# Kernel optimization log

Hardware: AMD Instinct MI355X
Metric: run time of the kernel (lower is better)

## Reference

```python
import jax, jax.numpy as jnp
import numpy as np

EPS = 1e-10
NCE_T = 0.1
JSD_T = 1.0

def setup_inputs() -> dict:
    key = jax.random.key(0)
    k1, k2, k3, k4, k5 = jax.random.split(key, 5)
    N, D, C = 8192, 128, 1000
    return {
        'fs': jax.random.normal(k1, (N, D), dtype=jnp.float32),
        'ft': jax.random.normal(k2, (N, D), dtype=jnp.float32),
        'logit_s': jax.random.normal(k3, (N, C), dtype=jnp.float32),
        'logit_t': jax.random.normal(k4, (N, C), dtype=jnp.float32),
        'target': jax.random.randint(k5, (N,), 0, 100, dtype=jnp.int64),
    }

def _l2_normalize(x, axis=1, eps=1e-12):
    n = jnp.sqrt(jnp.sum(x * x, axis=axis, keepdims=True))
    return x / jnp.maximum(n, eps)

def _nce_loss(f1, f2, targets):
    f1 = _l2_normalize(f1)
    f2 = _l2_normalize(f2)
    # pos_mask[i,j] = 1 where targets[i] == targets[j] (same class, incl. diagonal)
    pos_mask = (targets[:, None] == targets[None, :]).astype(jnp.float32)  # [N,N]
    neg_mask = 1.0 - pos_mask
    # dist = ||f1_i - f2_j||^2 = 2 - 2 <f1_i, f2_j> for unit vectors -> cos = 1 - 0.5*dist = f1 @ f2.T
    cos = jnp.matmul(f1, f2.T)  # [N,N]
    ps = jax.nn.softmax(cos / NCE_T, axis=1)
    log_pos = -jnp.log(ps + EPS) * pos_mask
    log_neg = -jnp.log(1.0 - ps + EPS) * neg_mask
    row = log_pos.sum(1) / pos_mask.sum(1) + log_neg.sum(1) / neg_mask.sum(1)
    return row.mean()

def _jsd_loss(y_s, y_t):
    N = y_s.shape[0]
    log_ps = jax.nn.log_softmax(y_s / JSD_T, axis=1)
    log_pt = jax.nn.log_softmax(y_t / JSD_T, axis=1)
    pt = jnp.exp(log_pt)
    ps = jnp.exp(log_ps)
    # F.kl_div(input=log_p, target=q, reduction='sum') = sum(q * (log q - log_p))
    kl_st = jnp.sum(pt * (log_pt - log_ps)) * (JSD_T ** 2) / N
    kl_ts = jnp.sum(ps * (log_ps - log_pt)) * (JSD_T ** 2) / N
    return 0.5 * (kl_st + kl_ts)

def reference(fs, ft, logit_s, logit_t, target):
    return _nce_loss(fs, ft, target) + _jsd_loss(logit_s, logit_t)
```

## Files before the change

kernel.cpp:

```cpp
#include <hip/hip_runtime.h>
#include <hip/hip_bf16.h>

#define NN 8192
#define DD 128
#define CC 1000
#define LN2 0.69314718f
#define G_SCALE 14.42695041f
#define NSTRIP 16
#define JPER   512
#define NTILE  8
#define LROW   128
#define GRID_MAIN 1024
#define RED_BLOCKS 32

typedef short v8s __attribute__((ext_vector_type(8)));
typedef float v4f __attribute__((ext_vector_type(4)));
typedef unsigned short u16;
typedef unsigned int u32;

typedef __attribute__((address_space(1))) const unsigned char ga_t;
typedef __attribute__((address_space(3))) unsigned char la_t;
#define GLOAD_LDS16(g, l) __builtin_amdgcn_global_load_lds((ga_t*)(g), (la_t*)(l), 16, 0, 0)

#if __has_builtin(__builtin_amdgcn_exp2f)
#define EXP2(x) __builtin_amdgcn_exp2f(x)
#else
#define EXP2(x) exp2f(x)
#endif
#if __has_builtin(__builtin_amdgcn_logf)
#define LOG2(x) __builtin_amdgcn_logf(x)
#else
#define LOG2(x) log2f(x)
#endif

static __device__ __forceinline__ float bf2f(u16 u) {
    union { float f; u32 i; } x; x.i = ((u32)u) << 16; return x.f;
}
static __device__ __forceinline__ u16 f2bf(float f) {
    u32 x = __float_as_uint(f);
    return (u16)((x + 0x7FFFu + ((x >> 16) & 1u)) >> 16);
}
static __device__ __forceinline__ float wsum(float v) {
    #pragma unroll
    for (int m = 1; m < 64; m <<= 1) v += __shfl_xor(v, m, 64);
    return v;
}
static __device__ __forceinline__ float wmax(float v) {
    #pragma unroll
    for (int m = 1; m < 64; m <<= 1) v = fmaxf(v, __shfl_xor(v, m, 64));
    return v;
}

__global__ __launch_bounds__(256) void prep_kernel(const void* __restrict__ fs,
                                                   const void* __restrict__ ft,
                                                   const int* __restrict__ traw,
                                                   u16* __restrict__ f1, u16* __restrict__ f2,
                                                   int* __restrict__ tgt32,
                                                   int* __restrict__ ghist,
                                                   float* __restrict__ sums) {
    __shared__ int h[128];
    int b = blockIdx.x, tid = threadIdx.x;
    int w = tid >> 6, lane = tid & 63;

    if (b < 1024) {
        #pragma unroll
        for (int r = 0; r < 4; r++) {
            int row4 = b * 16 + w * 4 + r;
            const void* src; u16* dst; float gain; int row;
            if (row4 < NN) { src = fs; dst = f1; gain = G_SCALE; row = row4; }
            else           { src = ft; dst = f2; gain = 1.0f;    row = row4 - NN; }
            u32 wb = ((const u32*)src)[(size_t)row * 64 + lane];
            unsigned e = (wb >> 7) & 0xFF;
            int isF32 = (__popcll(__ballot(e >= 100 && e <= 140)) < 32);
            float x0, x1;
            if (isF32) {
                float2 v = ((const float2*)src)[(size_t)row * 64 + lane];
                x0 = v.x; x1 = v.y;
            } else {
                x0 = bf2f((u16)(wb & 0xFFFF));
                x1 = bf2f((u16)(wb >> 16));
            }
            float ss = wsum(x0 * x0 + x1 * x1);
            float sc = gain / fmaxf(sqrtf(ss), 1e-12f);
            u32 outw = (u32)f2bf(x0 * sc) | ((u32)f2bf(x1 * sc) << 16);
            ((u32*)dst)[(size_t)row * 64 + lane] = outw;
        }
    } else {
        if (tid < 4) sums[tid] = 0.0f;
        if (tid < 128) h[tid] = 0;
        __syncthreads();
        for (int r = 0; r < 32; r++) {
            int idx = r * 256 + tid;
            int k = (idx >> 1) & 4095;
            int odd = traw[2 * k + 1];
            int is32 = (__ballot(odd != 0) != 0ull);
            int t = (is32 ? traw[idx] : traw[2 * idx]) & 127;
            tgt32[idx] = t;
            atomicAdd(&h[t], 1);
        }
        __syncthreads();
        if (tid < 128) ghist[tid] = h[tid];
    }
}

__global__ __launch_bounds__(256) void main_kernel(const u16* __restrict__ f1,
                                                   const u16* __restrict__ f2,
                                                   const int* __restrict__ tgt,
                                                   const void* __restrict__ ls,
                                                   const void* __restrict__ lt,
                                                   float* __restrict__ Pp,
                                                   float* __restrict__ Qp,
                                                   float* __restrict__ Sp,
                                                   float* __restrict__ sums) {
    __shared__ u16 lds[2][64 * LROW];
    __shared__ float sred[4];
    int bx = blockIdx.x;
    int tid = threadIdx.x;
    int w = tid >> 6, lane = tid & 63;

    {
        int strip = bx & (NSTRIP - 1);
        int ib = bx >> 4;
        int quad = lane >> 4, lcol = lane & 15;
        int ibase = ib * 128 + w * 32;

        v8s a0[4], a1[4];
        #pragma unroll
        for (int t = 0; t < 4; t++) {
            int k = t * 32 + quad * 8;
            a0[t] = *(const v8s*)(f1 + (size_t)(ibase + lcol) * DD + k);
            a1[t] = *(const v8s*)(f1 + (size_t)(ibase + 16 + lcol) * DD + k);
        }
        int ti[8];
        #pragma unroll
        for (int a = 0; a < 2; a++)
            #pragma unroll
            for (int v = 0; v < 4; v++)
                ti[a * 4 + v] = tgt[ibase + a * 16 + quad * 4 + v];

        float P[8] = {}, Q[8] = {}, S[8] = {};

        int rrl = 4 * w + (lane >> 4);
        int cg = (lane & 15) ^ rrl;
        const u16* gb = f2 + (size_t)strip * JPER * DD + (size_t)rrl * DD + cg * 8;
        int ldsbase = 4 * w * 256;

        #pragma unroll
        for (int r = 0; r < 4; r++)
            GLOAD_LDS16(gb + (size_t)r * 16 * DD,
                        (unsigned char*)lds[0] + ldsbase + r * 16 * 256);

        for (int it = 0; it < NTILE; ++it) {
            __syncthreads();
            if (it + 1 < NTILE) {
                const u16* g2 = gb + (size_t)(it + 1) * 64 * DD;
                unsigned char* l2 = (unsigned char*)lds[(it + 1) & 1] + ldsbase;
                #pragma unroll
                for (int r = 0; r < 4; r++)
                    GLOAD_LDS16(g2 + (size_t)r * 16 * DD, l2 + r * 16 * 256);
            }
            int jb = strip * JPER + it * 64;
            int tj0 = tgt[jb + lcol];
            int tj1 = tgt[jb + 16 + lcol];
            int tj2 = tgt[jb + 32 + lcol];
            int tj3 = tgt[jb + 48 + lcol];

            const u16* buf = lds[it & 1];
            v4f zero = {0.f, 0.f, 0.f, 0.f};
            v4f acc[8] = {zero, zero, zero, zero, zero, zero, zero, zero};
            #pragma unroll
            for (int t = 0; t < 4; t++) {
                int s = ((quad + 4 * t) ^ lcol) * 8;
                v8s b0 = *(const v8s*)(buf + (lcol)*LROW + s);
                v8s b1 = *(const v8s*)(buf + (16 + lcol) * LROW + s);
                v8s b2 = *(const v8s*)(buf + (32 + lcol) * LROW + s);
                v8s b3 = *(const v8s*)(buf + (48 + lcol) * LROW + s);
                acc[0] = __builtin_amdgcn_mfma_f32_16x16x32_bf16(a0[t], b0, acc[0], 0, 0, 0);
                acc[1] = __builtin_amdgcn_mfma_f32_16x16x32_bf16(a0[t], b1, acc[1], 0, 0, 0);
                acc[2] = __builtin_amdgcn_mfma_f32_16x16x32_bf16(a0[t], b2, acc[2], 0, 0, 0);
                acc[3] = __builtin_amdgcn_mfma_f32_16x16x32_bf16(a0[t], b3, acc[3], 0, 0, 0);
                acc[4] = __builtin_amdgcn_mfma_f32_16x16x32_bf16(a1[t], b0, acc[4], 0, 0, 0);
                acc[5] = __builtin_amdgcn_mfma_f32_16x16x32_bf16(a1[t], b1, acc[5], 0, 0, 0);
                acc[6] = __builtin_amdgcn_mfma_f32_16x16x32_bf16(a1[t], b2, acc[6], 0, 0, 0);
                acc[7] = __builtin_amdgcn_mfma_f32_16x16x32_bf16(a1[t], b3, acc[7], 0, 0, 0);
            }
            #pragma unroll
            for (int a = 0; a < 2; a++) {
                #pragma unroll
                for (int v = 0; v < 4; v++) {
                    int t_i = ti[a * 4 + v];
                    #pragma unroll
                    for (int jf = 0; jf < 4; jf++) {
                        float s2 = acc[a * 4 + jf][v];
                        float e1 = EXP2(s2);
                        int tj = (jf == 0) ? tj0 : (jf == 1) ? tj1 : (jf == 2) ? tj2 : tj3;
                        bool pos = (tj == t_i);
                        P[a * 4 + v] += e1;
                        Q[a * 4 + v] += pos ? e1 : 0.0f;
                        S[a * 4 + v] += pos ? s2 : 0.0f;
                    }
                }
            }
        }

        #pragma unroll
        for (int a = 0; a < 2; a++) {
            #pragma unroll
            for (int v = 0; v < 4; v++) {
                float p = P[a * 4 + v], q = Q[a * 4 + v], s = S[a * 4 + v];
                #pragma unroll
                for (int m = 1; m < 16; m <<= 1) {
                    p += __shfl_xor(p, m, 64);
                    q += __shfl_xor(q, m, 64);
                    s += __shfl_xor(s, m, 64);
                }
                if (lcol == 0) {
                    size_t idx = (size_t)strip * NN + ibase + a * 16 + quad * 4 + v;
                    Pp[idx] = p;
                    Qp[idx] = q;
                    Sp[idx] = s;
                }
            }
        }
    }

    float jacc = 0.0f;
    for (int jj = 0; jj < 2; jj++) {
        int row = bx * 8 + jj * 4 + w;
        u32 wb = ((const u32*)ls)[(size_t)row * 500 + lane];
        unsigned e = (wb >> 7) & 0xFF;
        int isF32 = (__popcll(__ballot(e >= 100 && e <= 140)) < 32);

        float xs[16], xt[16];
        #pragma unroll
        for (int c = 0; c < 4; c++) {
            int idx = c * 256 + lane * 4;
            if (idx < CC) {
                if (isF32) {
                    float4 a = *(const float4*)((const float*)ls + (size_t)row * CC + idx);
                    float4 bb = *(const float4*)((const float*)lt + (size_t)row * CC + idx);
                    xs[c*4+0] = a.x; xs[c*4+1] = a.y; xs[c*4+2] = a.z; xs[c*4+3] = a.w;
                    xt[c*4+0] = bb.x; xt[c*4+1] = bb.y; xt[c*4+2] = bb.z; xt[c*4+3] = bb.w;
                } else {
                    ushort4 a = *(const ushort4*)((const u16*)ls + (size_t)row * CC + idx);
                    ushort4 bb = *(const ushort4*)((const u16*)lt + (size_t)row * CC + idx);
                    xs[c*4+0] = bf2f(a.x); xs[c*4+1] = bf2f(a.y); xs[c*4+2] = bf2f(a.z); xs[c*4+3] = bf2f(a.w);
                    xt[c*4+0] = bf2f(bb.x); xt[c*4+1] = bf2f(bb.y); xt[c*4+2] = bf2f(bb.z); xt[c*4+3] = bf2f(bb.w);
                }
            } else {
                #pragma unroll
                for (int q = 0; q < 4; q++) { xs[c*4+q] = -1e30f; xt[c*4+q] = -1e30f; }
            }
        }
        #pragma unroll
        for (int q = 0; q < 16; q++) {
            asm volatile("" : "+v"(xs[q]));
            asm volatile("" : "+v"(xt[q]));
        }
        float ms = -1e30f, mt = -1e30f;
        #pragma unroll
        for (int q = 0; q < 16; q++) { ms = fmaxf(ms, xs[q]); mt = fmaxf(mt, xt[q]); }
        ms = wmax(ms); mt = wmax(mt);
        float es = 0.f, et = 0.f;
        #pragma unroll
        for (int q = 0; q < 16; q++) { es += __expf(xs[q] - ms); et += __expf(xt[q] - mt); }
        es = wsum(es); et = wsum(et);
        float lse_s = ms + __logf(es), lse_t = mt + __logf(et);
        float contrib = 0.f;
        #pragma unroll
        for (int q = 0; q < 16; q++) {
            float lps = xs[q] - lse_s, lpt = xt[q] - lse_t;
            contrib += (lpt - lps) * (__expf(lpt) - __expf(lps));
        }
        jacc += contrib;
    }
    jacc = wsum(jacc);
    if (lane == 0) sred[w] = jacc;
    __syncthreads();
    if (tid == 0) atomicAdd(&sums[1], sred[0] + sred[1] + sred[2] + sred[3]);
}

__global__ __launch_bounds__(256) void rowred_kernel(const float* __restrict__ Pp,
                                                     const float* __restrict__ Qp,
                                                     const float* __restrict__ Sp,
                                                     const int* __restrict__ tgt,
                                                     const int* __restrict__ ghist,
                                                     float* __restrict__ sums,
                                                     u32* __restrict__ out) {
    __shared__ float sb[4];
    __shared__ int lastf;
    int tid = threadIdx.x;

    int i = blockIdx.x * 256 + tid;
    float P = 0.f, Q = 0.f, S = 0.f;
    #pragma unroll
    for (int s = 0; s < NSTRIP; s++) {
        P += Pp[(size_t)s * NN + i];
        Q += Qp[(size_t)s * NN + i];
        S += Sp[(size_t)s * NN + i];
    }
    int cnt = ghist[tgt[i]];
    float pos = LN2 * LOG2(P) - LN2 * S / (float)cnt;
    float neg = (1.0f - Q / P) / (float)(NN - cnt);
    float l = wsum(pos + neg);
    if ((tid & 63) == 0) sb[tid >> 6] = l;
    __syncthreads();
    if (tid == 0) {
        atomicAdd(&sums[0], sb[0] + sb[1] + sb[2] + sb[3]);
        __threadfence();
        int* done = (int*)sums + 2;
        lastf = (atomicAdd(done, 1) == RED_BLOCKS - 1);
    }
    __syncthreads();
    if (!lastf) return;
    if (tid == 0) {
        float Lsum = __hip_atomic_load(&sums[0], __ATOMIC_RELAXED, __HIP_MEMORY_SCOPE_AGENT);
        float Jsum = __hip_atomic_load(&sums[1], __ATOMIC_RELAXED, __HIP_MEMORY_SCOPE_AGENT);
        float loss = (Lsum + 0.5f * Jsum) / (float)NN;
        u32 fb = __float_as_uint(loss);
        out[0] = (fb & 0xFFFF0000u) | (u32)f2bf(loss);
    }
}

extern "C" void kernel_launch(void* const* d_in, const int* in_sizes, int n_in,
                              void* d_out, int out_size, void* d_ws, size_t ws_size,
                              hipStream_t stream) {
    const void* fs = d_in[0];
    const void* ft = d_in[1];
    const void* ls = d_in[2];
    const void* lt = d_in[3];
    const int* tgt_raw = (const int*)d_in[4];

    char* wsp = (char*)d_ws;
    u16*   f1    = (u16*)(wsp + 0);
    u16*   f2    = (u16*)(wsp + 2097152);
    float* Pp    = (float*)(wsp + 4194304);
    float* Qp    = (float*)(wsp + 4718592);
    float* Sp    = (float*)(wsp + 5242880);
    float* sums  = (float*)(wsp + 5767168);
    int*   ghist = (int*)(wsp + 5767296);
    int*   tgt32 = (int*)(wsp + 5768192);

    prep_kernel<<<1025, 256, 0, stream>>>(fs, ft, tgt_raw, f1, f2, tgt32, ghist, sums);
    main_kernel<<<GRID_MAIN, 256, 0, stream>>>(f1, f2, tgt32, ls, lt, Pp, Qp, Sp, sums);
    rowred_kernel<<<RED_BLOCKS, 256, 0, stream>>>(Pp, Qp, Sp, tgt32, ghist, sums,
                                                  (u32*)d_out);
}
```

Baseline: 163.5 us.

## Interleave JSD row processing with NCE tile loop using online softmax

Moves the JSD logit work from a separate phase after the MFMA loop into the tile loop itself, processing one 256-column chunk per tile iteration. It uses an online (streaming) max/sum-exp formulation with a simplified KL identity (E_t[d] - E_s[d]), so each wave handles two rows across the eight iterations. Memory loads and exponentials for JSD can then overlap with the MFMA and LDS traffic, and the block-level LDS reduction is replaced by per-wave atomics. The trade-offs are extra rescaling exps per chunk, more atomics, and higher register pressure inside the main loop.

```diff
diff --git a/kernel.cpp b/kernel.cpp
--- a/kernel.cpp
+++ b/kernel.cpp
@@ -49,6 +49,12 @@
     #pragma unroll
     for (int m = 1; m < 64; m <<= 1) v = fmaxf(v, __shfl_xor(v, m, 64));
     return v;
+}
+static __device__ __forceinline__ float4 jload(const void* base, int row, int idx,
+                                               int isF32) {
+    if (isF32) return *(const float4*)((const float*)base + (size_t)row * CC + idx);
+    ushort4 v = *(const ushort4*)((const u16*)base + (size_t)row * CC + idx);
+    return make_float4(bf2f(v.x), bf2f(v.y), bf2f(v.z), bf2f(v.w));
 }
 
 __global__ __launch_bounds__(256) void prep_kernel(const void* __restrict__ fs,
@@ -113,171 +119,172 @@
                                                    float* __restrict__ Sp,
                                                    float* __restrict__ sums) {
     __shared__ u16 lds[2][64 * LROW];
-    __shared__ float sred[4];
     int bx = blockIdx.x;
     int tid = threadIdx.x;
     int w = tid >> 6, lane = tid & 63;
 
-    {
-        int strip = bx & (NSTRIP - 1);
-        int ib = bx >> 4;
-        int quad = lane >> 4, lcol = lane & 15;
-        int ibase = ib * 128 + w * 32;
-
-        v8s a0[4], a1[4];
+    int strip = bx & (NSTRIP - 1);
+    int ib = bx >> 4;
+    int quad = lane >> 4, lcol = lane & 15;
+    int ibase = ib * 128 + w * 32;
+
+    v8s a0[4], a1[4];
+    #pragma unroll
+    for (int t = 0; t < 4; t++) {
+        int k = t * 32 + quad * 8;
+        a0[t] = *(const v8s*)(f1 + (size_t)(ibase + lcol) * DD + k);
+        a1[t] = *(const v8s*)(f1 + (size_t)(ibase + 16 + lcol) * DD + k);
+    }
+    int ti[8];
+    #pragma unroll
+    for (int a = 0; a < 2; a++)
+        #pragma unroll
+        for (int v = 0; v < 4; v++)
+            ti[a * 4 + v] = tgt[ibase + a * 16 + quad * 4 + v];
+
+    float P[8] = {}, Q[8] = {}, S[8] = {};
+
+    int rA = bx * 8 + w * 2, rB = rA + 1;
+    u32 wbp = ((const u32*)ls)[(size_t)rA * 500 + lane];
+    unsigned exq = (wbp >> 7) & 0xFF;
+    int isF32 = (__popcll(__ballot(exq >= 100 && exq <= 140)) < 32);
+    float mS = -1e30f, eS = 0.f, uS = 0.f;
+    float mT = -1e30f, eT = 0.f, vT = 0.f;
+    float jc = 0.f;
+
+    int rrl = 4 * w + (lane >> 4);
+    int cg = (lane & 15) ^ rrl;
+    const u16* gb = f2 + (size_t)strip * JPER * DD + (size_t)rrl * DD + cg * 8;
+    int ldsbase = 4 * w * 256;
+
+    #pragma unroll
+    for (int r = 0; r < 4; r++)
+        GLOAD_LDS16(gb + (size_t)r * 16 * DD,
+                    (unsigned char*)lds[0] + ldsbase + r * 16 * 256);
+
+    for (int it = 0; it < NTILE; ++it) {
+        __syncthreads();
+        if (it + 1 < NTILE) {
+            const u16* g2 = gb + (size_t)(it + 1) * 64 * DD;
+            unsigned char* l2 = (unsigned char*)lds[(it + 1) & 1] + ldsbase;
+            #pragma unroll
+            for (int r = 0; r < 4; r++)
+                GLOAD_LDS16(g2 + (size_t)r * 16 * DD, l2 + r * 16 * 256);
+        }
+        int jb = strip * JPER + it * 64;
+        int tj0 = tgt[jb + lcol];
+        int tj1 = tgt[jb + 16 + lcol];
+        int tj2 = tgt[jb + 32 + lcol];
+        int tj3 = tgt[jb + 48 + lcol];
+
+        const u16* buf = lds[it & 1];
+        v4f zero = {0.f, 0.f, 0.f, 0.f};
+        v4f acc[8] = {zero, zero, zero, zero, zero, zero, zero, zero};
         #pragma unroll
         for (int t = 0; t < 4; t++) {
-            int k = t * 32 + quad * 8;
-            a0[t] = *(const v8s*)(f1 + (size_t)(ibase + lcol) * DD + k);
-            a1[t] = *(const v8s*)(f1 + (size_t)(ibase + 16 + lcol) * DD + k);
-        }
-        int ti[8];
-        #pragma unroll
-        for (int a = 0; a < 2; a++)
-            #pragma unroll
-            for (int v = 0; v < 4; v++)
-                ti[a * 4 + v] = tgt[ibase + a * 16 + quad * 4 + v];
-
-        float P[8] = {}, Q[8] = {}, S[8] = {};
-
-        int rrl = 4 * w + (lane >> 4);
-        int cg = (lane & 15) ^ rrl;
-        const u16* gb = f2 + (size_t)strip * JPER * DD + (size_t)rrl * DD + cg * 8;
-        int ldsbase = 4 * w * 256;
-
-        #pragma unroll
-        for (int r = 0; r < 4; r++)
-            GLOAD_LDS16(gb + (size_t)r * 16 * DD,
-                        (unsigned char*)lds[0] + ldsbase + r * 16 * 256);
-
-        for (int it = 0; it < NTILE; ++it) {
-            __syncthreads();
-            if (it + 1 < NTILE) {
-                const u16* g2 = gb + (size_t)(it + 1) * 64 * DD;
-                unsigned char* l2 = (unsigned char*)lds[(it + 1) & 1] + ldsbase;
-                #pragma unroll
-                for (int r = 0; r < 4; r++)
-                    GLOAD_LDS16(g2 + (size_t)r * 16 * DD, l2 + r * 16 * 256);
-            }
-            int jb = strip * JPER + it * 64;
-            int tj0 = tgt[jb + lcol];
-            int tj1 = tgt[jb + 16 + lcol];
-            int tj2 = tgt[jb + 32 + lcol];
-            int tj3 = tgt[jb + 48 + lcol];
-
-            const u16* buf = lds[it & 1];
-            v4f zero = {0.f, 0.f, 0.f, 0.f};
-            v4f acc[8] = {zero, zero, zero, zero, zero, zero, zero, zero};
-            #pragma unroll
-            for (int t = 0; t < 4; t++) {
-                int s = ((quad + 4 * t) ^ lcol) * 8;
-                v8s b0 = *(const v8s*)(buf + (lcol)*LROW + s);
-                v8s b1 = *(const v8s*)(buf + (16 + lcol) * LROW + s);
-                v8s b2 = *(const v8s*)(buf + (32 + lcol) * LROW + s);
-                v8s b3 = *(const v8s*)(buf + (48 + lcol) * LROW + s);
-                acc[0] = __builtin_amdgcn_mfma_f32_16x16x32_bf16(a0[t], b0, acc[0], 0, 0, 0);
-                acc[1] = __builtin_amdgcn_mfma_f32_16x16x32_bf16(a0[t], b1, acc[1], 0, 0, 0);
-                acc[2] = __builtin_amdgcn_mfma_f32_16x16x32_bf16(a0[t], b2, acc[2], 0, 0, 0);
-                acc[3] = __builtin_amdgcn_mfma_f32_16x16x32_bf16(a0[t], b3, acc[3], 0, 0, 0);
-                acc[4] = __builtin_amdgcn_mfma_f32_16x16x32_bf16(a1[t], b0, acc[4], 0, 0, 0);
-                acc[5] = __builtin_amdgcn_mfma_f32_16x16x32_bf16(a1[t], b1, acc[5], 0, 0, 0);
-                acc[6] = __builtin_amdgcn_mfma_f32_16x16x32_bf16(a1[t], b2, acc[6], 0, 0, 0);
-                acc[7] = __builtin_amdgcn_mfma_f32_16x16x32_bf16(a1[t], b3, acc[7], 0, 0, 0);
-            }
-            #pragma unroll
-            for (int a = 0; a < 2; a++) {
-                #pragma unroll
-                for (int v = 0; v < 4; v++) {
-                    int t_i = ti[a * 4 + v];
-                    #pragma unroll
-                    for (int jf = 0; jf < 4; jf++) {
-                        float s2 = acc[a * 4 + jf][v];
-                        float e1 = EXP2(s2);
-                        int tj = (jf == 0) ? tj0 : (jf == 1) ? tj1 : (jf == 2) ? tj2 : tj3;
-                        bool pos = (tj == t_i);
-                        P[a * 4 + v] += e1;
-                        Q[a * 4 + v] += pos ? e1 : 0.0f;
-                        S[a * 4 + v] += pos ? s2 : 0.0f;
-                    }
-                }
-            }
-        }
-
+            int s = ((quad + 4 * t) ^ lcol) * 8;
+            v8s b0 = *(const v8s*)(buf + (lcol)*LROW + s);
+            v8s b1 = *(const v8s*)(buf + (16 + lcol) * LROW + s);
+            v8s b2 = *(const v8s*)(buf + (32 + lcol) * LROW + s);
+            v8s b3 = *(const v8s*)(buf + (48 + lcol) * LROW + s);
+            acc[0] = __builtin_amdgcn_mfma_f32_16x16x32_bf16(a0[t], b0, acc[0], 0, 0, 0);
+            acc[1] = __builtin_amdgcn_mfma_f32_16x16x32_bf16(a0[t], b1, acc[1], 0, 0, 0);
+            acc[2] = __builtin_amdgcn_mfma_f32_16x16x32_bf16(a0[t], b2, acc[2], 0, 0, 0);
+            acc[3] = __builtin_amdgcn_mfma_f32_16x16x32_bf16(a0[t], b3, acc[3], 0, 0, 0);
+            acc[4] = __builtin_amdgcn_mfma_f32_16x16x32_bf16(a1[t], b0, acc[4], 0, 0, 0);
+            acc[5] = __builtin_amdgcn_mfma_f32_16x16x32_bf16(a1[t], b1, acc[5], 0, 0, 0);
+            acc[6] = __builtin_amdgcn_mfma_f32_16x16x32_bf16(a1[t], b2, acc[6], 0, 0, 0);
+            acc[7] = __builtin_amdgcn_mfma_f32_16x16x32_bf16(a1[t], b3, acc[7], 0, 0, 0);
+        }
         #pragma unroll
         for (int a = 0; a < 2; a++) {
             #pragma unroll
             for (int v = 0; v < 4; v++) {
-                float p = P[a * 4 + v], q = Q[a * 4 + v], s = S[a * 4 + v];
+                int t_i = ti[a * 4 + v];
                 #pragma unroll
-                for (int m = 1; m < 16; m <<= 1) {
-                    p += __shfl_xor(p, m, 64);
-                    q += __shfl_xor(q, m, 64);
-                    s += __shfl_xor(s, m, 64);
+                for (int jf = 0; jf < 4; jf++) {
+                    float s2 = acc[a * 4 + jf][v];
+                    float e1 = EXP2(s2);
+                    int tj = (jf == 0) ? tj0 : (jf == 1) ? tj1 : (jf == 2) ? tj2 : tj3;
+                    bool pos = (tj == t_i);
+                    P[a * 4 + v] += e1;
+                    Q[a * 4 + v] += pos ? e1 : 0.0f;
+                    S[a * 4 + v] += pos ? s2 : 0.0f;
                 }
-                if (lcol == 0) {
-                    size_t idx = (size_t)strip * NN + ibase + a * 16 + quad * 4 + v;
-                    Pp[idx] = p;
-                    Qp[idx] = q;
-                    Sp[idx] = s;
-                }
-            }
-        }
-    }
-
-    float jacc = 0.0f;
-    for (int jj = 0; jj < 2; jj++) {
-        int row = bx * 8 + jj * 4 + w;
-        u32 wb = ((const u32*)ls)[(size_t)row * 500 + lane];
-        unsigned e = (wb >> 7) & 0xFF;
-        int isF32 = (__popcll(__ballot(e >= 100 && e <= 140)) < 32);
-
-        float xs[16], xt[16];
-        #pragma unroll
-        for (int c = 0; c < 4; c++) {
+            }
+        }
+
+        {
+            int c = it & 3;
+            int row = (it < 4) ? rA : rB;
             int idx = c * 256 + lane * 4;
+            float x0, x1, x2, x3, y0, y1, y2, y3;
             if (idx < CC) {
-                if (isF32) {
-                    float4 a = *(const float4*)((const float*)ls + (size_t)row * CC + idx);
-                    float4 bb = *(const float4*)((const float*)lt + (size_t)row * CC + idx);
-                    xs[c*4+0] = a.x; xs[c*4+1] = a.y; xs[c*4+2] = a.z; xs[c*4+3] = a.w;
-                    xt[c*4+0] = bb.x; xt[c*4+1] = bb.y; xt[c*4+2] = bb.z; xt[c*4+3] = bb.w;
-                } else {
-                    ushort4 a = *(const ushort4*)((const u16*)ls + (size_t)row * CC + idx);
-                    ushort4 bb = *(const ushort4*)((const u16*)lt + (size_t)row * CC + idx);
-                    xs[c*4+0] = bf2f(a.x); xs[c*4+1] = bf2f(a.y); xs[c*4+2] = bf2f(a.z); xs[c*4+3] = bf2f(a.w);
-                    xt[c*4+0] = bf2f(bb.x); xt[c*4+1] = bf2f(bb.y); xt[c*4+2] = bf2f(bb.z); xt[c*4+3] = bf2f(bb.w);
-                }
+                float4 xv = jload(ls, row, idx, isF32);
+                float4 yv = jload(lt, row, idx, isF32);
+                x0 = xv.x; x1 = xv.y; x2 = xv.z; x3 = xv.w;
+                y0 = yv.x; y1 = yv.y; y2 = yv.z; y3 = yv.w;
             } else {
-                #pragma unroll
-                for (int q = 0; q < 4; q++) { xs[c*4+q] = -1e30f; xt[c*4+q] = -1e30f; }
-            }
-        }
-        #pragma unroll
-        for (int q = 0; q < 16; q++) {
-            asm volatile("" : "+v"(xs[q]));
-            asm volatile("" : "+v"(xt[q]));
-        }
-        float ms = -1e30f, mt = -1e30f;
-        #pragma unroll
-        for (int q = 0; q < 16; q++) { ms = fmaxf(ms, xs[q]); mt = fmaxf(mt, xt[q]); }
-        ms = wmax(ms); mt = wmax(mt);
-        float es = 0.f, et = 0.f;
-        #pragma unroll
-        for (int q = 0; q < 16; q++) { es += __expf(xs[q] - ms); et += __expf(xt[q] - mt); }
-        es = wsum(es); et = wsum(et);
-        float lse_s = ms + __logf(es), lse_t = mt + __logf(et);
-        float contrib = 0.f;
-        #pragma unroll
-        for (int q = 0; q < 16; q++) {
-            float lps = xs[q] - lse_s, lpt = xt[q] - lse_t;
-            contrib += (lpt - lps) * (__expf(lpt) - __expf(lps));
-        }
-        jacc += contrib;
-    }
-    jacc = wsum(jacc);
-    if (lane == 0) sred[w] = jacc;
-    __syncthreads();
-    if (tid == 0) atomicAdd(&sums[1], sred[0] + sred[1] + sred[2] + sred[3]);
+                x0 = x1 = x2 = x3 = -1e30f;
+                y0 = y1 = y2 = y3 = -1e30f;
+            }
+            float d0 = y0 - x0, d1 = y1 - x1, d2 = y2 - x2, d3 = y3 - x3;
+            {
+                float cm = fmaxf(fmaxf(x0, x1), fmaxf(x2, x3));
+                float t0 = __expf(x0 - cm), t1 = __expf(x1 - cm);
+                float t2 = __expf(x2 - cm), t3 = __expf(x3 - cm);
+                float ce = t0 + t1 + t2 + t3;
+                float cu = d0 * t0 + d1 * t1 + d2 * t2 + d3 * t3;
+                float nm = fmaxf(mS, cm);
+                float sa = __expf(mS - nm), sb = __expf(cm - nm);
+                eS = eS * sa + ce * sb;
+                uS = uS * sa + cu * sb;
+                mS = nm;
+            }
+            {
+                float cm = fmaxf(fmaxf(y0, y1), fmaxf(y2, y3));
+                float t0 = __expf(y0 - cm), t1 = __expf(y1 - cm);
+                float t2 = __expf(y2 - cm), t3 = __expf(y3 - cm);
+                float ce = t0 + t1 + t2 + t3;
+                float cv = d0 * t0 + d1 * t1 + d2 * t2 + d3 * t3;
+                float nm = fmaxf(mT, cm);
+                float sa = __expf(mT - nm), sb = __expf(cm - nm);
+                eT = eT * sa + ce * sb;
+                vT = vT * sa + cv * sb;
+                mT = nm;
+            }
+            if (c == 3) {
+                float MS = wmax(mS), MT = wmax(mT);
+                float ws_ = __expf(mS - MS), wt_ = __expf(mT - MT);
+                float ES = wsum(eS * ws_), US = wsum(uS * ws_);
+                float ET = wsum(eT * wt_), VT = wsum(vT * wt_);
+                jc += VT / ET - US / ES;
+                mS = mT = -1e30f; eS = eT = uS = vT = 0.f;
+            }
+        }
+    }
+
+    #pragma unroll
+    for (int a = 0; a < 2; a++) {
+        #pragma unroll
+        for (int v = 0; v < 4; v++) {
+            float p = P[a * 4 + v], q = Q[a * 4 + v], s = S[a * 4 + v];
+            #pragma unroll
+            for (int m = 1; m < 16; m <<= 1) {
+                p += __shfl_xor(p, m, 64);
+                q += __shfl_xor(q, m, 64);
+                s += __shfl_xor(s, m, 64);
+            }
+            if (lcol == 0) {
+                size_t idx = (size_t)strip * NN + ibase + a * 16 + quad * 4 + v;
+                Pp[idx] = p;
+                Qp[idx] = q;
+                Sp[idx] = s;
+            }
+        }
+    }
+
+    if (lane == 0) atomicAdd(&sums[1], jc);
 }
 
 __global__ __launch_bounds__(256) void rowred_kernel(const float* __restrict__ Pp,
```

Measured after the change: 188.6 us. 1.15x slower.
